# Kernel optimization log

Hardware: AMD Instinct MI355X
Metric: run time of the kernel (lower is better)

## Reference

```python
import jax, jax.numpy as jnp
import numpy as np

# par: dt=0.05, tau_m=10.0 -> alpha = 1 - dt/tau_m; v_th = 2.0
ALPHA = 1.0 - 0.05 / 10.0
V_TH = 2.0


def setup_inputs() -> dict:
    key = jax.random.key(0)
    k1, k2 = jax.random.split(key)
    B, T, N = 128, 1000, 1024
    x = jax.random.normal(k1, (B, T, N), dtype=jnp.float32)
    # torch init: normal(mean=0, std=1/sqrt(N))
    w = jax.random.normal(k2, (N,), dtype=jnp.float32) * (1.0 / np.sqrt(N))
    return {"x": x, "w": w}


def reference(x, w):
    """Runs the NeuronClass.__call__ LIF step over all T timesteps.

    v_t = alpha * v_{t-1} + x_t @ w - v_th * stop_grad(z_{t-1})
    z_t = 1[v_t - v_th > 0]
    Returns (v_seq, z_seq), each [B, T].
    """
    B, T, N = x.shape
    # Precompute the input current for all timesteps (same math as per-step x_t @ w,
    # but a single large GEMM instead of T small GEMVs).
    drive = jnp.einsum('btn,n->bt', x, w)  # [B, T]

    def step(carry, i_t):
        v, z = carry
        v = ALPHA * v + i_t - V_TH * jax.lax.stop_gradient(z)
        z = (v - V_TH > 0).astype(v.dtype)
        return (v, z), (v, z)

    v0 = jnp.zeros((B,), dtype=x.dtype)
    z0 = jnp.zeros((B,), dtype=x.dtype)
    _, (v_seq, z_seq) = jax.lax.scan(step, (v0, z0), drive.T)  # scanned outputs [T, B]
    return v_seq.T, z_seq.T
```

## Files before the change

### kernel.cpp

```cpp
#include <hip/hip_runtime.h>


#define ALPHA 0.995f
#define V_TH 2.0f

constexpr int B = 128;
constexpr int T = 1000;
constexpr int N = 1024;

__global__ __launch_bounds__(256) void lif_dot_kernel(
    const float* __restrict__ x, const float* __restrict__ w,
    float* __restrict__ drive_t) {
    const int lane = threadIdx.x & 63;
    const int gwave = blockIdx.x * 4 + (threadIdx.x >> 6);
    const int base_row = gwave * 16;

    const float* wp = w + lane * 4;
    const float4 w0 = *(const float4*)(wp);
    const float4 w1 = *(const float4*)(wp + 256);
    const float4 w2 = *(const float4*)(wp + 512);
    const float4 w3 = *(const float4*)(wp + 768);

    for (int i = 0; i < 16; i += 2) {
        const float* xr0 = x + (long long)(base_row + i) * N + lane * 4;
        const float* xr1 = xr0 + N;
        const float4 a0 = *(const float4*)(xr0);
        const float4 a1 = *(const float4*)(xr0 + 256);
        const float4 a2 = *(const float4*)(xr0 + 512);
        const float4 a3 = *(const float4*)(xr0 + 768);
        const float4 b0 = *(const float4*)(xr1);
        const float4 b1 = *(const float4*)(xr1 + 256);
        const float4 b2 = *(const float4*)(xr1 + 512);
        const float4 b3 = *(const float4*)(xr1 + 768);

        double s0 = (double)a0.x*w0.x + (double)a0.y*w0.y + (double)a0.z*w0.z + (double)a0.w*w0.w;
        double s1 = (double)a1.x*w1.x + (double)a1.y*w1.y + (double)a1.z*w1.z + (double)a1.w*w1.w;
        double s2 = (double)a2.x*w2.x + (double)a2.y*w2.y + (double)a2.z*w2.z + (double)a2.w*w2.w;
        double s3 = (double)a3.x*w3.x + (double)a3.y*w3.y + (double)a3.z*w3.z + (double)a3.w*w3.w;
        double t0 = (double)b0.x*w0.x + (double)b0.y*w0.y + (double)b0.z*w0.z + (double)b0.w*w0.w;
        double t1 = (double)b1.x*w1.x + (double)b1.y*w1.y + (double)b1.z*w1.z + (double)b1.w*w1.w;
        double t2 = (double)b2.x*w2.x + (double)b2.y*w2.y + (double)b2.z*w2.z + (double)b2.w*w2.w;
        double t3 = (double)b3.x*w3.x + (double)b3.y*w3.y + (double)b3.z*w3.z + (double)b3.w*w3.w;
        double accA = (s0 + s1) + (s2 + s3);
        double accB = (t0 + t1) + (t2 + t3);

#pragma unroll
        for (int off = 32; off >= 1; off >>= 1) {
            accA += __shfl_down(accA, off);
            accB += __shfl_down(accB, off);
        }

        if (lane == 0) {
            const int row = base_row + i;
            const int b = row / T;
            const int t = row - b * T;
            drive_t[t * B + b] = (float)accA;
            const int row2 = row + 1;
            const int b2 = row2 / T;
            const int t2 = row2 - b2 * T;
            drive_t[t2 * B + b2] = (float)accB;
        }
    }
}

__global__ __launch_bounds__(256) void lif_scan_kernel(
    const float* __restrict__ drive_t, float* __restrict__ out) {
    constexpr int TT = 50;
    constexpr int BB = 64;
    __shared__ float s_drive[TT][BB];
    __shared__ float s_v[BB][TT + 1];
    __shared__ float s_z[BB][TT + 1];

    const int tid = threadIdx.x;
    const int b0 = blockIdx.x * BB;
    const int jload = tid >> 6;
    const int bload = tid & 63;

    float v = 0.0f, z = 0.0f;

    for (int t0 = 0; t0 < T; t0 += TT) {
        for (int j = jload; j < TT; j += 4)
            s_drive[j][bload] = drive_t[(t0 + j) * B + b0 + bload];
        __syncthreads();

        if (tid < BB) {
#pragma unroll
            for (int j = 0; j < TT; ++j) {
                const float d = s_drive[j][tid];
                v = ALPHA * v + d - V_TH * z;
                z = (v - V_TH > 0.0f) ? 1.0f : 0.0f;
                s_v[tid][j] = v;
                s_z[tid][j] = z;
            }
        }
        __syncthreads();

        for (int idx = tid; idx < BB * TT; idx += 256) {
            const int bb = idx / TT;
            const int j = idx - bb * TT;
            out[(long long)(b0 + bb) * T + t0 + j] = s_v[bb][j];
        }
        for (int idx = tid; idx < BB * TT; idx += 256) {
            const int bb = idx / TT;
            const int j = idx - bb * TT;
            out[(long long)B * T + (long long)(b0 + bb) * T + t0 + j] = s_z[bb][j];
        }
    }
}

extern "C" void kernel_launch(void* const* d_in, const int* in_sizes, int n_in,
                              void* d_out, int out_size, void* d_ws, size_t ws_size,
                              hipStream_t stream) {
    const float* x = (const float*)d_in[0];
    const float* w = (const float*)d_in[1];
    float* out = (float*)d_out;
    float* drive_t = (float*)d_ws;

    lif_dot_kernel<<<2000, 256, 0, stream>>>(x, w, drive_t);
    lif_scan_kernel<<<2, 256, 0, stream>>>(drive_t, out);
}
```

Measured before the change: 807.8 us.

## Use nontemporal loads, more waves in dot kernel, single-block vectorized scan

New measurement: 686.5 us. 1.18x faster.

```diff
diff --git a/kernel.cpp b/kernel.cpp
--- a/kernel.cpp
+++ b/kernel.cpp
@@ -8,30 +8,33 @@
 constexpr int T = 1000;
 constexpr int N = 1024;
 
+typedef float f32x4 __attribute__((ext_vector_type(4)));
+
 __global__ __launch_bounds__(256) void lif_dot_kernel(
     const float* __restrict__ x, const float* __restrict__ w,
     float* __restrict__ drive_t) {
     const int lane = threadIdx.x & 63;
     const int gwave = blockIdx.x * 4 + (threadIdx.x >> 6);
-    const int base_row = gwave * 16;
+    const int base_row = gwave * 4;
 
     const float* wp = w + lane * 4;
-    const float4 w0 = *(const float4*)(wp);
-    const float4 w1 = *(const float4*)(wp + 256);
-    const float4 w2 = *(const float4*)(wp + 512);
-    const float4 w3 = *(const float4*)(wp + 768);
+    const f32x4 w0 = *(const f32x4*)(wp);
+    const f32x4 w1 = *(const f32x4*)(wp + 256);
+    const f32x4 w2 = *(const f32x4*)(wp + 512);
+    const f32x4 w3 = *(const f32x4*)(wp + 768);
 
-    for (int i = 0; i < 16; i += 2) {
-        const float* xr0 = x + (long long)(base_row + i) * N + lane * 4;
-        const float* xr1 = xr0 + N;
-        const float4 a0 = *(const float4*)(xr0);
-        const float4 a1 = *(const float4*)(xr0 + 256);
-        const float4 a2 = *(const float4*)(xr0 + 512);
-        const float4 a3 = *(const float4*)(xr0 + 768);
-        const float4 b0 = *(const float4*)(xr1);
-        const float4 b1 = *(const float4*)(xr1 + 256);
-        const float4 b2 = *(const float4*)(xr1 + 512);
-        const float4 b3 = *(const float4*)(xr1 + 768);
+#pragma unroll
+    for (int i = 0; i < 4; i += 2) {
+        const f32x4* xr0 = (const f32x4*)(x + (long long)(base_row + i) * N + lane * 4);
+        const f32x4* xr1 = (const f32x4*)((const float*)xr0 + N);
+        const f32x4 a0 = __builtin_nontemporal_load(xr0);
+        const f32x4 a1 = __builtin_nontemporal_load(xr0 + 64);
+        const f32x4 a2 = __builtin_nontemporal_load(xr0 + 128);
+        const f32x4 a3 = __builtin_nontemporal_load(xr0 + 192);
+        const f32x4 b0 = __builtin_nontemporal_load(xr1);
+        const f32x4 b1 = __builtin_nontemporal_load(xr1 + 64);
+        const f32x4 b2 = __builtin_nontemporal_load(xr1 + 128);
+        const f32x4 b3 = __builtin_nontemporal_load(xr1 + 192);
 
         double s0 = (double)a0.x*w0.x + (double)a0.y*w0.y + (double)a0.z*w0.z + (double)a0.w*w0.w;
         double s1 = (double)a1.x*w1.x + (double)a1.y*w1.y + (double)a1.z*w1.z + (double)a1.w*w1.w;
@@ -52,59 +55,58 @@
 
         if (lane == 0) {
             const int row = base_row + i;
-            const int b = row / T;
-            const int t = row - b * T;
-            drive_t[t * B + b] = (float)accA;
+            const int b1_ = row / T;
+            const int t1_ = row - b1_ * T;
+            drive_t[t1_ * B + b1_] = (float)accA;
             const int row2 = row + 1;
-            const int b2 = row2 / T;
-            const int t2 = row2 - b2 * T;
-            drive_t[t2 * B + b2] = (float)accB;
+            const int b2_ = row2 / T;
+            const int t2_ = row2 - b2_ * T;
+            drive_t[t2_ * B + b2_] = (float)accB;
         }
     }
 }
 
-__global__ __launch_bounds__(256) void lif_scan_kernel(
+__global__ __launch_bounds__(512) void lif_scan_kernel(
     const float* __restrict__ drive_t, float* __restrict__ out) {
-    constexpr int TT = 50;
-    constexpr int BB = 64;
-    __shared__ float s_drive[TT][BB];
-    __shared__ float s_v[BB][TT + 1];
-    __shared__ float s_z[BB][TT + 1];
-
+    __shared__ float s_drive[64 * B];
+    __shared__ float s_v[B][65];
+    __shared__ float s_z[B][65];
     const int tid = threadIdx.x;
-    const int b0 = blockIdx.x * BB;
-    const int jload = tid >> 6;
-    const int bload = tid & 63;
 
     float v = 0.0f, z = 0.0f;
+    for (int t0 = 0; t0 < T; t0 += 64) {
+        const int TT = (T - t0 < 64) ? (T - t0) : 64;
+        const int nq = (TT * B) / 4;
 
-    for (int t0 = 0; t0 < T; t0 += TT) {
-        for (int j = jload; j < TT; j += 4)
-            s_drive[j][bload] = drive_t[(t0 + j) * B + b0 + bload];
+        const f32x4* src = (const f32x4*)(drive_t + t0 * B);
+        f32x4* dst = (f32x4*)s_drive;
+        for (int idx = tid; idx < nq; idx += 512)
+            dst[idx] = src[idx];
         __syncthreads();
 
-        if (tid < BB) {
-#pragma unroll
+        if (tid < B) {
+            float vv = v, zz = z;
             for (int j = 0; j < TT; ++j) {
-                const float d = s_drive[j][tid];
-                v = ALPHA * v + d - V_TH * z;
-                z = (v - V_TH > 0.0f) ? 1.0f : 0.0f;
-                s_v[tid][j] = v;
-                s_z[tid][j] = z;
+                const float d = s_drive[j * B + tid];
+                vv = ALPHA * vv + d - V_TH * zz;
+                zz = (vv - V_TH > 0.0f) ? 1.0f : 0.0f;
+                s_v[tid][j] = vv;
+                s_z[tid][j] = zz;
             }
+            v = vv; z = zz;
         }
         __syncthreads();
 
-        for (int idx = tid; idx < BB * TT; idx += 256) {
-            const int bb = idx / TT;
-            const int j = idx - bb * TT;
-            out[(long long)(b0 + bb) * T + t0 + j] = s_v[bb][j];
+        const int qpb = TT / 4;
+        for (int idx = tid; idx < nq; idx += 512) {
+            const int bb = idx / qpb;
+            const int j4 = (idx - bb * qpb) * 4;
+            f32x4 vq = { s_v[bb][j4], s_v[bb][j4+1], s_v[bb][j4+2], s_v[bb][j4+3] };
+            *(f32x4*)(out + (long long)bb * T + t0 + j4) = vq;
+            f32x4 zq = { s_z[bb][j4], s_z[bb][j4+1], s_z[bb][j4+2], s_z[bb][j4+3] };
+            *(f32x4*)(out + (long long)(B + bb) * T + t0 + j4) = zq;
         }
-        for (int idx = tid; idx < BB * TT; idx += 256) {
-            const int bb = idx / TT;
-            const int j = idx - bb * TT;
-            out[(long long)B * T + (long long)(b0 + bb) * T + t0 + j] = s_z[bb][j];
-        }
+        __syncthreads();
     }
 }
 
@@ -116,6 +118,6 @@
     float* out = (float*)d_out;
     float* drive_t = (float*)d_ws;
 
-    lif_dot_kernel<<<2000, 256, 0, stream>>>(x, w, drive_t);
-    lif_scan_kernel<<<2, 256, 0, stream>>>(drive_t, out);
+    lif_dot_kernel<<<8000, 256, 0, stream>>>(x, w, drive_t);
+    lif_scan_kernel<<<1, 512, 0, stream>>>(drive_t, out);
 }
```
